# Performance work log

Measured on AMD Instinct MI355X. Metric: run time of the kernel, lower is better.

The kernel has to match this reference:

```python
import jax, jax.numpy as jnp
import numpy as np

IN_SIZE, OUT_SIZE, EDGE_SIZE = 32, 32, 16
NET_LAYERS = [128, 128]          # cfg.net_layers (hidden sizes of the edge MLP)
B, N_NEIGH = 10000, 20           # nodes x neighbors
E = B * N_NEIGH                  # total edges


def setup_inputs() -> dict:
    key = jax.random.key(0)
    ks = jax.random.split(key, 16)
    h_v = jax.random.normal(ks[0], (B, N_NEIGH), jnp.float32)
    h_w = jax.random.normal(ks[1], (B, IN_SIZE), jnp.float32)
    e_vw = jax.random.normal(ks[2], (E, EDGE_SIZE), jnp.float32)
    dims = [EDGE_SIZE] + NET_LAYERS + [IN_SIZE * OUT_SIZE]
    params = {}
    for i, (din, dout) in enumerate(zip(dims[:-1], dims[1:])):
        bound = 1.0 / np.sqrt(din)  # torch nn.Linear default init
        params[f"W{i}"] = jax.random.uniform(ks[3 + 2 * i], (dout, din), jnp.float32, -bound, bound)
        params[f"b{i}"] = jax.random.uniform(ks[4 + 2 * i], (dout,), jnp.float32, -bound, bound)
    return {"h_v": h_v, "h_w": h_w, "e_vw": e_vw, **params}


def reference(h_v, h_w, e_vw, W0, b0, W1, b1, W2, b2):
    # Edge MLP: edge_size -> 128 -> 128 -> in*out (ReLU on hidden layers only)
    x = jax.nn.relu(e_vw @ W0.T + b0)
    x = jax.nn.relu(x @ W1.T + b1)
    m = (x @ W2.T + b2).reshape(-1, OUT_SIZE, IN_SIZE)  # [E, out, in]

    # Faithful reproduction of h_w[..., None].expand(B, in, n).view(-1, in)
    n = h_v.shape[1]
    h_w_rows = jnp.broadcast_to(h_w[:, :, None], (h_w.shape[0], IN_SIZE, n)).reshape(-1, IN_SIZE)  # [E, in]

    # bmm(m, h_w_rows[..., None]).squeeze() -> [E, out]
    out = jnp.einsum("eoi,ei->eo", m, h_w_rows)
    return jnp.squeeze(out)
```

## Files before the change

kernel.cpp:

```cpp
#include <hip/hip_runtime.h>


typedef __bf16 bf16x8 __attribute__((ext_vector_type(8)));
typedef float  f32x4  __attribute__((ext_vector_type(4)));

#define NB       10000
#define NNEIGH   20
#define PADH     136
#define NCHUNK   25

#define WS_W0S   0
#define WS_W1B   8192
#define WS_W2G   40960
#define WS_B2G   532480

__device__ __forceinline__ unsigned short f2bf(float f) {
    unsigned int u = __float_as_uint(f);
    unsigned int r = (u + 0x7fffu + ((u >> 16) & 1u)) >> 16;
    return (unsigned short)r;
}
__device__ __forceinline__ unsigned int pack2(float a, float b) {
    return (unsigned int)f2bf(a) | ((unsigned int)f2bf(b) << 16);
}

__global__ __launch_bounds__(256) void prep_kernel(
    const float* __restrict__ W0, const float* __restrict__ b0,
    const float* __restrict__ W1,
    const float* __restrict__ W2, const float* __restrict__ b2,
    unsigned short* __restrict__ w0s, unsigned short* __restrict__ w1b,
    unsigned short* __restrict__ w2g, float* __restrict__ b2g)
{
    const int bx = blockIdx.x, tid = threadIdx.x;
    if (bx < 16) {
        int gid = bx * 256 + tid;
        int o = gid >> 7, k = gid & 127;
        float pref[32];
        float run = 0.f;
#pragma unroll
        for (int i = 0; i < 32; ++i) {
            run += W2[(size_t)(32 * o + i) * 128 + k];
            pref[i] = run;
        }
#pragma unroll
        for (int kn = 0; kn < 20; ++kn) {
            const int j0 = (32 * kn) / 20;
#pragma unroll
            for (int g = 0; g < 3; ++g) {
                int lo = 20 * (j0 + g) - 32 * kn;     if (lo < 0) lo = 0;
                int hi = 20 * (j0 + g + 1) - 32 * kn; if (hi > 32) hi = 32;
                float v = (hi > lo) ? (pref[hi - 1] - (lo > 0 ? pref[lo - 1] : 0.f)) : 0.f;
                w2g[((size_t)(kn * 3 + g) * 32 + o) * 128 + k] = f2bf(v);
            }
        }
    } else if (bx == 16) {
        for (int t = 0; t < 16; ++t) {
            int idx = t * 256 + tid;
            int ct = idx >> 9, lane = (idx >> 3) & 63, j = idx & 7;
            int lq = lane & 15, q = lane >> 4;
            int k = q * 8 + j, o = ct * 16 + lq;
            float v = (k < 16) ? W0[o * 16 + k] : (k == 16 ? b0[o] : 0.f);
            w0s[idx] = f2bf(v);
        }
    } else if (bx <= 32) {
        int base = (bx - 17) * 1024;
        for (int i2 = tid; i2 < 1024; i2 += 256)
            w1b[base + i2] = f2bf(W1[base + i2]);
    } else {
        for (int idx = tid; idx < 1920; idx += 256) {
            int kn = idx / 96, rem = idx - kn * 96;
            int g = rem >> 5, o = rem & 31;
            int j0 = (32 * kn) / 20;
            int lo = 20 * (j0 + g) - 32 * kn;     if (lo < 0) lo = 0;
            int hi = 20 * (j0 + g + 1) - 32 * kn; if (hi > 32) hi = 32;
            float s = 0.f;
            for (int i = lo; i < hi; ++i) s += b2[32 * o + i];
            b2g[idx] = s;
        }
    }
}

__global__ __launch_bounds__(256) void msg_kernel(
    const float* __restrict__ h_w, const float* __restrict__ e_vw,
    const float* __restrict__ b1v,
    const unsigned short* __restrict__ w0s, const unsigned short* __restrict__ w1b,
    const unsigned short* __restrict__ w2g, const float* __restrict__ b2g,
    float* __restrict__ out)
{
    __shared__ __align__(16) unsigned short sW1[128 * PADH];
    __shared__ __align__(16) unsigned short sW2g[96 * PADH];
    __shared__ __align__(16) unsigned short sX[64 * PADH];

    const int tid = threadIdx.x;
    const int lane = tid & 63, w = tid >> 6;
    const int quad = lane >> 4, lq = lane & 15;
    const int kn = blockIdx.y, chunk = blockIdx.x;
    const int j0 = (32 * kn) / 20;

    {
        const uint4* src = (const uint4*)w1b;
        uint4* dst = (uint4*)sW1;
        for (int i = tid; i < 2048; i += 256) { int r = i >> 4, c = i & 15; dst[r * 17 + c] = src[i]; }
    }
    {
        const uint4* src = (const uint4*)(w2g + (size_t)kn * 96 * 128);
        uint4* dst = (uint4*)sW2g;
        for (int i = tid; i < 1536; i += 256) { int r = i >> 4, c = i & 15; dst[r * 17 + c] = src[i]; }
    }

    bf16x8 w0f[8];
#pragma unroll
    for (int ct = 0; ct < 8; ++ct)
        w0f[ct] = *(const bf16x8*)(w0s + (ct * 64 + lane) * 8);
    float4 b1r4[8];
#pragma unroll
    for (int ct = 0; ct < 8; ++ct)
        b1r4[ct] = *(const float4*)(b1v + ct * 16 + quad * 4);
    float4 b2r4[6];
#pragma unroll
    for (int ct = 0; ct < 6; ++ct)
        b2r4[ct] = *(const float4*)(b2g + kn * 96 + ct * 16 + quad * 4);
    __syncthreads();

    const int rbase = w * 16;
    const unsigned short one_bf = 0x3f80;

    for (int btile = chunk; btile < 157; btile += NCHUNK) {
        const int bbase = btile * 64;
        const int e = bbase + rbase + lq;

        union { bf16x8 v; uint4 u; } B;
        B.u = make_uint4(0u, 0u, 0u, 0u);
        if (quad < 2) {
            if (e < NB) {
                const float4* p = (const float4*)(e_vw + ((size_t)e * NNEIGH + kn) * 16 + quad * 8);
                float4 f0 = p[0], f1 = p[1];
                B.u = make_uint4(pack2(f0.x, f0.y), pack2(f0.z, f0.w),
                                 pack2(f1.x, f1.y), pack2(f1.z, f1.w));
            }
        } else if (quad == 2) {
            B.u.x = (unsigned int)one_bf;
        }

        float hwv[3];
#pragma unroll
        for (int g = 0; g < 3; ++g) {
            int jv = j0 + g; if (jv > 31) jv = 31;
            hwv[g] = (e < NB) ? h_w[e * 32 + jv] : 0.f;
        }

#pragma unroll
        for (int ct = 0; ct < 8; ++ct) {
            f32x4 acc = {0.f, 0.f, 0.f, 0.f};
            acc = __builtin_amdgcn_mfma_f32_16x16x32_bf16(w0f[ct], B.v, acc, 0, 0, 0);
#pragma unroll
            for (int r2 = 0; r2 < 4; ++r2) acc[r2] = acc[r2] > 0.f ? acc[r2] : 0.f;
            uint2 pk = make_uint2(pack2(acc[0], acc[1]), pack2(acc[2], acc[3]));
            *(uint2*)&sX[(rbase + lq) * PADH + ct * 16 + quad * 4] = pk;
        }

        {
            bf16x8 xf[4];
#pragma unroll
            for (int ka = 0; ka < 4; ++ka)
                xf[ka] = *(const bf16x8*)&sX[(rbase + lq) * PADH + ka * 32 + quad * 8];
#pragma unroll
            for (int ct = 0; ct < 8; ++ct) {
                f32x4 acc = {b1r4[ct].x, b1r4[ct].y, b1r4[ct].z, b1r4[ct].w};
#pragma unroll
                for (int ka = 0; ka < 4; ++ka) {
                    bf16x8 wf = *(const bf16x8*)&sW1[(ct * 16 + lq) * PADH + ka * 32 + quad * 8];
                    acc = __builtin_amdgcn_mfma_f32_16x16x32_bf16(wf, xf[ka], acc, 0, 0, 0);
                }
#pragma unroll
                for (int r2 = 0; r2 < 4; ++r2) acc[r2] = acc[r2] > 0.f ? acc[r2] : 0.f;
                uint2 pk = make_uint2(pack2(acc[0], acc[1]), pack2(acc[2], acc[3]));
                *(uint2*)&sX[(rbase + lq) * PADH + ct * 16 + quad * 4] = pk;
            }
        }

        {
            bf16x8 xf[4];
#pragma unroll
            for (int ka = 0; ka < 4; ++ka)
                xf[ka] = *(const bf16x8*)&sX[(rbase + lq) * PADH + ka * 32 + quad * 8];
            f32x4 accC[6];
#pragma unroll
            for (int ct = 0; ct < 6; ++ct) {
                f32x4 acc = {b2r4[ct].x, b2r4[ct].y, b2r4[ct].z, b2r4[ct].w};
#pragma unroll
                for (int ka = 0; ka < 4; ++ka) {
                    bf16x8 wf = *(const bf16x8*)&sW2g[(ct * 16 + lq) * PADH + ka * 32 + quad * 8];
                    acc = __builtin_amdgcn_mfma_f32_16x16x32_bf16(wf, xf[ka], acc, 0, 0, 0);
                }
                accC[ct] = acc;
            }
            if (e < NB) {
#pragma unroll
                for (int half = 0; half < 2; ++half) {
                    float4 val;
                    float* vp = &val.x;
#pragma unroll
                    for (int r2 = 0; r2 < 4; ++r2) {
                        float s = 0.f;
#pragma unroll
                        for (int g = 0; g < 3; ++g)
                            s += hwv[g] * accC[g * 2 + half][r2];
                        vp[r2] = s;
                    }
                    *(float4*)(out + ((size_t)e * NNEIGH + kn) * 32 + half * 16 + quad * 4) = val;
                }
            }
        }
    }
}

extern "C" void kernel_launch(void* const* d_in, const int* in_sizes, int n_in,
                              void* d_out, int out_size, void* d_ws, size_t ws_size,
                              hipStream_t stream)
{
    const float* h_w = (const float*)d_in[1];
    const float* e_vw = (const float*)d_in[2];
    const float* W0 = (const float*)d_in[3];
    const float* b0 = (const float*)d_in[4];
    const float* W1 = (const float*)d_in[5];
    const float* b1 = (const float*)d_in[6];
    const float* W2 = (const float*)d_in[7];
    const float* b2 = (const float*)d_in[8];
    float* out = (float*)d_out;

    char* ws = (char*)d_ws;
    unsigned short* w0s = (unsigned short*)(ws + WS_W0S);
    unsigned short* w1b = (unsigned short*)(ws + WS_W1B);
    unsigned short* w2g = (unsigned short*)(ws + WS_W2G);
    float*          b2g = (float*)(ws + WS_B2G);

    prep_kernel<<<34, 256, 0, stream>>>(W0, b0, W1, W2, b2, w0s, w1b, w2g, b2g);
    dim3 grid(NCHUNK, 20);
    msg_kernel<<<grid, 256, 0, stream>>>(h_w, e_vw, b1, w0s, w1b, w2g, b2g, out);
}
```

Measured before the change: 136.7 us.

## Prefetch next tile's edge and h_w inputs and pre-gather h_w into coalesced layout

The prep kernel gains extra blocks that gather h_w into a per-(neighbor, group) transposed array, so the message kernel reads it with coalesced loads. The message kernel software-pipelines its loop, loading the next tile's e_vw features and h_w values while computing the current tile. Bias vectors move from registers to shared memory, and launch bounds request 2 blocks per SM, to lower register pressure. The cost is an extra 2.4MB gather pass and more global traffic in the prep kernel.

```diff
diff --git a/kernel.cpp b/kernel.cpp
--- a/kernel.cpp
+++ b/kernel.cpp
@@ -13,6 +13,7 @@
 #define WS_W1B   8192
 #define WS_W2G   40960
 #define WS_B2G   532480
+#define WS_HWG   540160
 
 __device__ __forceinline__ unsigned short f2bf(float f) {
     unsigned int u = __float_as_uint(f);
@@ -27,8 +28,10 @@
     const float* __restrict__ W0, const float* __restrict__ b0,
     const float* __restrict__ W1,
     const float* __restrict__ W2, const float* __restrict__ b2,
+    const float* __restrict__ h_w,
     unsigned short* __restrict__ w0s, unsigned short* __restrict__ w1b,
-    unsigned short* __restrict__ w2g, float* __restrict__ b2g)
+    unsigned short* __restrict__ w2g, float* __restrict__ b2g,
+    float* __restrict__ hwg)
 {
     const int bx = blockIdx.x, tid = threadIdx.x;
     if (bx < 16) {
@@ -65,7 +68,7 @@
         int base = (bx - 17) * 1024;
         for (int i2 = tid; i2 < 1024; i2 += 256)
             w1b[base + i2] = f2bf(W1[base + i2]);
-    } else {
+    } else if (bx == 33) {
         for (int idx = tid; idx < 1920; idx += 256) {
             int kn = idx / 96, rem = idx - kn * 96;
             int g = rem >> 5, o = rem & 31;
@@ -76,11 +79,22 @@
             for (int i = lo; i < hi; ++i) s += b2[32 * o + i];
             b2g[idx] = s;
         }
-    }
-}
-
-__global__ __launch_bounds__(256) void msg_kernel(
-    const float* __restrict__ h_w, const float* __restrict__ e_vw,
+    } else {
+#pragma unroll
+        for (int t = 0; t < 4; ++t) {
+            int idx = (bx - 34) * 1024 + t * 256 + tid;
+            if (idx < 600000) {
+                int kn3 = idx / 10000, b = idx - kn3 * 10000;
+                int kn = kn3 / 3, g = kn3 - kn * 3;
+                int jv = (32 * kn) / 20 + g; if (jv > 31) jv = 31;
+                hwg[idx] = h_w[b * 32 + jv];
+            }
+        }
+    }
+}
+
+__global__ __launch_bounds__(256, 2) void msg_kernel(
+    const float* __restrict__ hwg, const float* __restrict__ e_vw,
     const float* __restrict__ b1v,
     const unsigned short* __restrict__ w0s, const unsigned short* __restrict__ w1b,
     const unsigned short* __restrict__ w2g, const float* __restrict__ b2g,
@@ -89,12 +103,13 @@
     __shared__ __align__(16) unsigned short sW1[128 * PADH];
     __shared__ __align__(16) unsigned short sW2g[96 * PADH];
     __shared__ __align__(16) unsigned short sX[64 * PADH];
+    __shared__ __align__(16) float sB1[128];
+    __shared__ __align__(16) float sB2G[96];
 
     const int tid = threadIdx.x;
     const int lane = tid & 63, w = tid >> 6;
     const int quad = lane >> 4, lq = lane & 15;
     const int kn = blockIdx.y, chunk = blockIdx.x;
-    const int j0 = (32 * kn) / 20;
 
     {
         const uint4* src = (const uint4*)w1b;
@@ -106,46 +121,56 @@
         uint4* dst = (uint4*)sW2g;
         for (int i = tid; i < 1536; i += 256) { int r = i >> 4, c = i & 15; dst[r * 17 + c] = src[i]; }
     }
+    if (tid < 128) sB1[tid] = b1v[tid];
+    if (tid < 96)  sB2G[tid] = b2g[kn * 96 + tid];
 
     bf16x8 w0f[8];
 #pragma unroll
     for (int ct = 0; ct < 8; ++ct)
         w0f[ct] = *(const bf16x8*)(w0s + (ct * 64 + lane) * 8);
-    float4 b1r4[8];
-#pragma unroll
-    for (int ct = 0; ct < 8; ++ct)
-        b1r4[ct] = *(const float4*)(b1v + ct * 16 + quad * 4);
-    float4 b2r4[6];
-#pragma unroll
-    for (int ct = 0; ct < 6; ++ct)
-        b2r4[ct] = *(const float4*)(b2g + kn * 96 + ct * 16 + quad * 4);
     __syncthreads();
 
     const int rbase = w * 16;
     const unsigned short one_bf = 0x3f80;
 
+    float4 f0, f1;
+    float hwv[3];
+    {
+        const int e = chunk * 64 + rbase + lq;
+        if (quad < 2 && e < NB) {
+            const float4* p = (const float4*)(e_vw + ((size_t)e * NNEIGH + kn) * 16 + quad * 8);
+            f0 = p[0]; f1 = p[1];
+        }
+#pragma unroll
+        for (int g = 0; g < 3; ++g)
+            hwv[g] = (e < NB) ? hwg[(kn * 3 + g) * NB + e] : 0.f;
+    }
+
     for (int btile = chunk; btile < 157; btile += NCHUNK) {
-        const int bbase = btile * 64;
-        const int e = bbase + rbase + lq;
+        const int e = btile * 64 + rbase + lq;
 
         union { bf16x8 v; uint4 u; } B;
         B.u = make_uint4(0u, 0u, 0u, 0u);
         if (quad < 2) {
-            if (e < NB) {
-                const float4* p = (const float4*)(e_vw + ((size_t)e * NNEIGH + kn) * 16 + quad * 8);
-                float4 f0 = p[0], f1 = p[1];
+            if (e < NB)
                 B.u = make_uint4(pack2(f0.x, f0.y), pack2(f0.z, f0.w),
                                  pack2(f1.x, f1.y), pack2(f1.z, f1.w));
-            }
         } else if (quad == 2) {
             B.u.x = (unsigned int)one_bf;
         }
-
-        float hwv[3];
-#pragma unroll
-        for (int g = 0; g < 3; ++g) {
-            int jv = j0 + g; if (jv > 31) jv = 31;
-            hwv[g] = (e < NB) ? h_w[e * 32 + jv] : 0.f;
+        float hw0 = hwv[0], hw1 = hwv[1], hw2 = hwv[2];
+
+        {
+            const int ne = (btile + NCHUNK) * 64 + rbase + lq;
+            if (btile + NCHUNK < 157) {
+                if (quad < 2 && ne < NB) {
+                    const float4* p = (const float4*)(e_vw + ((size_t)ne * NNEIGH + kn) * 16 + quad * 8);
+                    f0 = p[0]; f1 = p[1];
+                }
+#pragma unroll
+                for (int g = 0; g < 3; ++g)
+                    hwv[g] = (ne < NB) ? hwg[(kn * 3 + g) * NB + ne] : 0.f;
+            }
         }
 
 #pragma unroll
@@ -165,7 +190,7 @@
                 xf[ka] = *(const bf16x8*)&sX[(rbase + lq) * PADH + ka * 32 + quad * 8];
 #pragma unroll
             for (int ct = 0; ct < 8; ++ct) {
-                f32x4 acc = {b1r4[ct].x, b1r4[ct].y, b1r4[ct].z, b1r4[ct].w};
+                f32x4 acc = *(const f32x4*)&sB1[ct * 16 + quad * 4];
 #pragma unroll
                 for (int ka = 0; ka < 4; ++ka) {
                     bf16x8 wf = *(const bf16x8*)&sW1[(ct * 16 + lq) * PADH + ka * 32 + quad * 8];
@@ -186,7 +211,7 @@
             f32x4 accC[6];
 #pragma unroll
             for (int ct = 0; ct < 6; ++ct) {
-                f32x4 acc = {b2r4[ct].x, b2r4[ct].y, b2r4[ct].z, b2r4[ct].w};
+                f32x4 acc = *(const f32x4*)&sB2G[ct * 16 + quad * 4];
 #pragma unroll
                 for (int ka = 0; ka < 4; ++ka) {
                     bf16x8 wf = *(const bf16x8*)&sW2g[(ct * 16 + lq) * PADH + ka * 32 + quad * 8];
@@ -200,13 +225,9 @@
                     float4 val;
                     float* vp = &val.x;
 #pragma unroll
-                    for (int r2 = 0; r2 < 4; ++r2) {
-                        float s = 0.f;
-#pragma unroll
-                        for (int g = 0; g < 3; ++g)
-                            s += hwv[g] * accC[g * 2 + half][r2];
-                        vp[r2] = s;
-                    }
+                    for (int r2 = 0; r2 < 4; ++r2)
+                        vp[r2] = hw0 * accC[half][r2] + hw1 * accC[2 + half][r2]
+                               + hw2 * accC[4 + half][r2];
                     *(float4*)(out + ((size_t)e * NNEIGH + kn) * 32 + half * 16 + quad * 4) = val;
                 }
             }
@@ -233,8 +254,10 @@
     unsigned short* w1b = (unsigned short*)(ws + WS_W1B);
     unsigned short* w2g = (unsigned short*)(ws + WS_W2G);
     float*          b2g = (float*)(ws + WS_B2G);
-
-    prep_kernel<<<34, 256, 0, stream>>>(W0, b0, W1, W2, b2, w0s, w1b, w2g, b2g);
+    float*          hwg = (float*)(ws + WS_HWG);
+
+    prep_kernel<<<34 + 586, 256, 0, stream>>>(W0, b0, W1, W2, b2, h_w,
+                                              w0s, w1b, w2g, b2g, hwg);
     dim3 grid(NCHUNK, 20);
-    msg_kernel<<<grid, 256, 0, stream>>>(h_w, e_vw, b1, w0s, w1b, w2g, b2g, out);
-}
+    msg_kernel<<<grid, 256, 0, stream>>>(hwg, e_vw, b1, w0s, w1b, w2g, b2g, out);
+}
```

New measurement: 184.7 us. 1.35x slower.
